# Kernel tuning notes

Measured on AMD Instinct MI355X. Metric: run time of the kernel, lower is better.

Reference implementation:

```python
import jax, jax.numpy as jnp
import numpy as np

B, F, D, V = 8192, 26, 32, 100000
H1, H2 = 128, 128  # cin_size
U1, U2 = 400, 400  # dnn hidden units


def setup_inputs() -> dict:
    key = jax.random.key(0)
    ks = jax.random.split(key, 12)
    s = 0.05  # keep activations/sigmoid in a sane range
    return {
        "dense_inputs": jax.random.normal(ks[0], (B, 13), jnp.float32),
        "sparse_inputs": jax.random.randint(ks[1], (B, F), 0, V, jnp.int32),
        "E": jax.random.normal(ks[2], (F, V, D), jnp.float32) * s,
        "W_cin0": jax.random.normal(ks[3], (F, F, H1), jnp.float32) * s,
        "W_cin1": jax.random.normal(ks[4], (F, H1, H2), jnp.float32) * s,
        "W1": jax.random.normal(ks[5], (F * D, U1), jnp.float32) * s,
        "b1": jnp.zeros((U1,), jnp.float32),
        "W2": jax.random.normal(ks[6], (U1, U2), jnp.float32) * s,
        "b2": jnp.zeros((U2,), jnp.float32),
        "w_lin": jax.random.normal(ks[7], (F, 1), jnp.float32) * s,
        "b_lin": jnp.zeros((1,), jnp.float32),
        "w_out": jax.random.normal(ks[8], (1 + H1 + H2 + U2 + 13, 1), jnp.float32) * s,
        "b_out": jnp.zeros((1,), jnp.float32),
    }


def reference(dense_inputs, sparse_inputs, E, W_cin0, W_cin1, W1, b1, W2, b2,
              w_lin, b_lin, w_out, b_out):
    # Linear part: Dense(1) applied to raw (cast) sparse ids, as in the TF code.
    linear_out = sparse_inputs.astype(jnp.float32) @ w_lin + b_lin  # [B,1]

    # Embedding lookup: per-field tables. embed[b,f,:] = E[f, sparse[b,f], :]
    embed = E[jnp.arange(F)[None, :], sparse_inputs]  # [B,F,D]

    # CIN. The split->matmul->reshape->conv1d chain is exactly:
    #   x_{k+1}[b,h,d] = sum_{i,j} W_k[i,j,h] * X0[b,i,d] * x_k[b,j,d]
    X0 = embed
    x1 = jnp.einsum('bid,bjd,ijh->bhd', X0, X0, W_cin0)   # [B,H1,D]
    x2 = jnp.einsum('bid,bjd,ijh->bhd', X0, x1, W_cin1)   # [B,H2,D]
    cin_out = jnp.concatenate([x1, x2], axis=1).sum(axis=-1)  # [B,H1+H2]

    # DNN on flattened embeddings (dropout rate 0 -> identity at inference).
    v = embed.reshape(B, F * D)
    h = jax.nn.relu(v @ W1 + b1)
    h = jax.nn.relu(h @ W2 + b2)  # [B,U2]

    total = jnp.concatenate([linear_out, cin_out, h, dense_inputs], axis=-1)
    return jax.nn.sigmoid(total @ w_out + b_out)  # [B,1]
```

## Files before the change

kernel.cpp:

```cpp
#include <hip/hip_runtime.h>
#include <hip/hip_bf16.h>
#include <math.h>

typedef __attribute__((ext_vector_type(8))) short bf16x8;
typedef __attribute__((ext_vector_type(4))) float f32x4;

#define B_ 8192
#define F_ 26
#define D_ 32
#define V_ 100000
#define NP_ 351
#define KP_ 352

static const size_t OFF_VB    = 0;
static const size_t OFF_LIN   = 13631488;
static const size_t OFF_CIN1  = 13664256;
static const size_t OFF_CIN2P = 17858560;
static const size_t OFF_G     = 34635776;
static const size_t OFF_H1B   = 89161728;
static const size_t OFF_H2    = 95715328;
static const size_t OFF_W0T   = 108822528;
static const size_t OFF_WC1T  = 108912640;
static const size_t OFF_W1T   = 109764608;
static const size_t OFF_W2T   = 110430208;

static __device__ __forceinline__ unsigned short f2b(float f) {
    unsigned int u = __float_as_uint(f);
    return (unsigned short)((u + 0x7FFF + ((u >> 16) & 1)) >> 16);
}
static __device__ __forceinline__ unsigned short f2bt(float f) {
    return (unsigned short)(__float_as_uint(f) >> 16);
}
static __device__ __forceinline__ unsigned int pk2t(float a, float b) {
    return __builtin_amdgcn_perm(__float_as_uint(b), __float_as_uint(a), 0x07060302u);
}
static __device__ __forceinline__ float bf2f(unsigned short u) {
    return __uint_as_float(((unsigned int)u) << 16);
}

static __device__ __forceinline__ void transpose_body(
    const float* __restrict__ src, unsigned short* __restrict__ dst,
    int K, int N, int bx, int by)
{
    __shared__ float tl[32][33];
    const int lx = threadIdx.x & 31, ly = threadIdx.x >> 5;
    const int n0 = bx * 32, k0 = by * 32;
#pragma unroll
    for (int i = 0; i < 4; ++i) {
        int k = k0 + ly + i * 8, n = n0 + lx;
        if (k < K && n < N) tl[ly + i * 8][lx] = src[(size_t)k * N + n];
    }
    __syncthreads();
#pragma unroll
    for (int i = 0; i < 4; ++i) {
        int n = n0 + ly + i * 8, k = k0 + lx;
        if (k < K && n < N) dst[(size_t)n * K + k] = f2b(tl[lx][ly + i * 8]);
    }
}

__global__ __launch_bounds__(256) void k0_all(
    const float* __restrict__ W0, const float* __restrict__ Wc1,
    const float* __restrict__ W1, const float* __restrict__ W2,
    unsigned short* __restrict__ W0t, unsigned short* __restrict__ Wc1t,
    unsigned short* __restrict__ W1t, unsigned short* __restrict__ W2t)
{
    int bid = blockIdx.x;
    if (bid < 176) {
        int g = bid * 256 + threadIdx.x;
        if (g < 128 * KP_) {
            int h = g / KP_, p = g % KP_;
            float w = 0.f;
            if (p < NP_) {
                int i = 0, base = 0;
                while (base + (F_ - i) <= p) { base += F_ - i; ++i; }
                int j = i + (p - base);
                w = W0[(i * F_ + j) * 128 + h];
                if (i != j) w += W0[(j * F_ + i) * 128 + h];
            }
            W0t[g] = f2b(w);
        }
        return;
    }
    bid -= 176;
    const float* src; unsigned short* dst; int K, N, nx;
    if (bid < 416)               { src = Wc1; dst = Wc1t; K = 3328; N = 128; nx = 4; }
    else if ((bid -= 416) < 338) { src = W1;  dst = W1t;  K = 832;  N = 400; nx = 13; }
    else                         { bid -= 338; src = W2; dst = W2t; K = 400; N = 400; nx = 13; }
    transpose_body(src, dst, K, N, bid % nx, bid / nx);
}

__global__ __launch_bounds__(256) void k1_embed_cin(
    const int*   __restrict__ sparse,
    const float* __restrict__ E,
    const unsigned short* __restrict__ W0t,
    const float* __restrict__ wlin,
    const float* __restrict__ blin,
    unsigned short* __restrict__ vb,
    float* __restrict__ lin,
    float* __restrict__ cin1,
    unsigned short* __restrict__ G)
{
    __shared__ __align__(16) unsigned short embB[32][40];
    __shared__ __align__(16) unsigned short P[32][360];
    __shared__ __align__(16) unsigned short x1s[128][40];
    __shared__ float cin1t[2][128];
    __shared__ float linb[F_];
    __shared__ int   idxs[F_];
    __shared__ unsigned char pI[KP_], pJ[KP_];

    const int b = blockIdx.x, t = threadIdx.x;

    if (t < F_) {
        int id = sparse[b * F_ + t];
        idxs[t] = id;
        linb[t] = (float)id * wlin[t];
        int i = t, base = F_ * i - (i * (i - 1)) / 2;
        for (int j = i; j < F_; ++j) { pI[base + j - i] = (unsigned char)i; pJ[base + j - i] = (unsigned char)j; }
    }
    __syncthreads();

    if (t < 208) {
        int f = t >> 3, q = t & 7;
        float4 r = *(const float4*)(E + ((size_t)f * V_ + idxs[f]) * D_ + q * 4);
        uint2 uu;
        uu.x = pk2t(r.x, r.y);
        uu.y = pk2t(r.z, r.w);
        *(uint2*)&embB[f][q * 4] = uu;
        *(uint2*)(vb + (size_t)b * 832 + f * 32 + q * 4) = uu;
    }
    if (t >= 208 && t < 208 + 96) {
        int o = t - 208;
        *(unsigned int*)&embB[26 + (o >> 4)][(o & 15) * 2] = 0u;
    }
    __syncthreads();

    {
        const int d = t & 31, pb = t >> 5;
        const int p0 = pb * 44;
        for (int k = 0; k < 22; ++k) {
            int p = p0 + 2 * k;
            float a  = bf2f(embB[pI[p]][d]) * bf2f(embB[pJ[p]][d]);
            float c2 = (p + 1 < NP_) ? bf2f(embB[pI[p + 1]][d]) * bf2f(embB[pJ[p + 1]][d]) : 0.f;
            *(unsigned int*)&P[d][p] = pk2t(a, c2);
        }
        if (t == 0) { float s = blin[0]; for (int f = 0; f < F_; ++f) s += linb[f]; lin[b] = s; }
    }
    __syncthreads();

    const int wave = t >> 6, lane = t & 63;
    const int lr = lane & 15, lg = lane >> 4;
    const int mt = wave & 1, ntb = (wave >> 1) * 4;
    f32x4 acc[4] = {};
    {
        const unsigned short* Arow = &P[mt * 16 + lr][lg * 8];
        for (int kt = 0; kt < 11; ++kt) {
            bf16x8 af = *(const bf16x8*)(Arow + kt * 32);
#pragma unroll
            for (int n = 0; n < 4; ++n) {
                const unsigned short* bp = W0t + (size_t)((ntb + n) * 16 + lr) * KP_ + kt * 32 + lg * 8;
                bf16x8 bfg = *(const bf16x8*)bp;
                acc[n] = __builtin_amdgcn_mfma_f32_16x16x32_bf16(af, bfg, acc[n], 0, 0, 0);
            }
        }
    }
#pragma unroll
    for (int n = 0; n < 4; ++n) {
        float s = acc[n][0] + acc[n][1] + acc[n][2] + acc[n][3];
        s += __shfl_xor(s, 16, 64);
        s += __shfl_xor(s, 32, 64);
        int h = (ntb + n) * 16 + lr;
        if (lg == 0) cin1t[mt][h] = s;
        int d0 = mt * 16 + lg * 4;
        *(unsigned int*)&x1s[h][d0]     = pk2t(acc[n][0], acc[n][1]);
        *(unsigned int*)&x1s[h][d0 + 2] = pk2t(acc[n][2], acc[n][3]);
    }
    __syncthreads();

    if (t < 128) cin1[(size_t)b * 128 + t] = cin1t[0][t] + cin1t[1][t];

    {
        bf16x8 ea = *(const bf16x8*)&embB[mt * 16 + lr][lg * 8];
#pragma unroll
        for (int n = 0; n < 4; ++n) {
            bf16x8 xb = *(const bf16x8*)&x1s[(ntb + n) * 16 + lr][lg * 8];
            f32x4 g = {};
            g = __builtin_amdgcn_mfma_f32_16x16x32_bf16(ea, xb, g, 0, 0, 0);
            int j = (ntb + n) * 16 + lr;
            int i0 = mt * 16 + lg * 4;
#pragma unroll
            for (int r = 0; r < 4; ++r) {
                int i = i0 + r;
                if (i < F_) G[(size_t)b * 3328 + i * 128 + j] = f2bt(g[r]);
            }
        }
    }
}

static __device__ __forceinline__ void gemm_body(
    const unsigned short* __restrict__ A, int lda, int kbase,
    const unsigned short* __restrict__ Bt, int ldb, int N,
    const float* __restrict__ bias, bool relu, bool outb,
    void* __restrict__ C, int ldc, int m0, int n0,
    unsigned short (*As)[40], unsigned short (*Bs)[40])
{
    const int t = threadIdx.x;
    const int wave = t >> 6, lane = t & 63;
    const int lr = lane & 15, lg = lane >> 4;
    const int wn = wave * 32;
    const int ar = t >> 2, kg = (t & 3) * 8;

    const unsigned short* aptr = A  + (size_t)(m0 + ar) * lda + kbase + kg;
    const unsigned short* bp0  = Bt + (size_t)(n0 + ar) * ldb + kbase + kg;
    const unsigned short* bp1  = Bt + (size_t)(n0 + 64 + ar) * ldb + kbase + kg;
    const bool bn0 = (n0 + ar) < N, bn1 = (n0 + 64 + ar) < N;

    const uint4 z4 = make_uint4(0u, 0u, 0u, 0u);
    uint4 av  = *(const uint4*)aptr;
    uint4 bv0 = bn0 ? *(const uint4*)bp0 : z4;
    uint4 bv1 = bn1 ? *(const uint4*)bp1 : z4;

    f32x4 acc[4][2] = {};
    for (int kt = 0; kt < 26; ++kt) {
        *(uint4*)&As[ar][kg]      = av;
        *(uint4*)&Bs[ar][kg]      = bv0;
        *(uint4*)&Bs[64 + ar][kg] = bv1;
        __syncthreads();
        if (kt + 1 < 26) {
            av  = *(const uint4*)(aptr + (kt + 1) * 32);
            bv0 = bn0 ? *(const uint4*)(bp0 + (kt + 1) * 32) : z4;
            bv1 = bn1 ? *(const uint4*)(bp1 + (kt + 1) * 32) : z4;
        }
        bf16x8 af[4], bfr[2];
#pragma unroll
        for (int i = 0; i < 4; ++i) af[i]  = *(const bf16x8*)&As[i * 16 + lr][lg * 8];
#pragma unroll
        for (int j = 0; j < 2; ++j) bfr[j] = *(const bf16x8*)&Bs[wn + j * 16 + lr][lg * 8];
#pragma unroll
        for (int i = 0; i < 4; ++i)
#pragma unroll
            for (int j = 0; j < 2; ++j)
                acc[i][j] = __builtin_amdgcn_mfma_f32_16x16x32_bf16(af[i], bfr[j], acc[i][j], 0, 0, 0);
        __syncthreads();
    }
#pragma unroll
    for (int i = 0; i < 4; ++i) {
        int mrow = m0 + i * 16 + lg * 4;
#pragma unroll
        for (int j = 0; j < 2; ++j) {
            int col = n0 + wn + j * 16 + lr;
            if (col >= N) continue;
            float bb = bias ? bias[col] : 0.f;
#pragma unroll
            for (int r = 0; r < 4; ++r) {
                float vv = acc[i][j][r] + bb;
                if (relu) vv = fmaxf(vv, 0.f);
                if (outb) ((unsigned short*)C)[(size_t)(mrow + r) * ldc + col] = f2bt(vv);
                else      ((float*)C)[(size_t)(mrow + r) * ldc + col] = vv;
            }
        }
    }
}

__global__ __launch_bounds__(256) void k2_h1_cin2(
    const unsigned short* __restrict__ vb, const unsigned short* __restrict__ W1t,
    const float* __restrict__ b1, unsigned short* __restrict__ h1b,
    const unsigned short* __restrict__ G, const unsigned short* __restrict__ Wc1t,
    float* __restrict__ cin2p)
{
    __shared__ __align__(16) unsigned short As[64][40];
    __shared__ __align__(16) unsigned short Bs[128][40];
    const int m0 = blockIdx.y * 64;
    if (blockIdx.z == 0) {
        gemm_body(vb, 832, 0, W1t, 832, 400, b1, true, true, h1b, 400,
                  m0, blockIdx.x * 128, As, Bs);
    } else {
        float* Cp = cin2p + (size_t)blockIdx.x * B_ * 128;
        gemm_body(G, 3328, blockIdx.x * 832, Wc1t, 3328, 128, nullptr, false, false, Cp, 128,
                  m0, 0, As, Bs);
    }
}

__global__ __launch_bounds__(256) void k2_h2(
    const unsigned short* __restrict__ A, const unsigned short* __restrict__ Bt,
    const float* __restrict__ bias, float* __restrict__ C)
{
    __shared__ __align__(16) unsigned short As[64][40];
    __shared__ __align__(16) unsigned short Bs[128][40];
    const int t = threadIdx.x;
    const int m0 = blockIdx.y * 64, n0 = blockIdx.x * 128;
    const int N = 400, K = 400, ld = 400;
    const int wave = t >> 6, lane = t & 63;
    const int lr = lane & 15, lg = lane >> 4;
    const int wn = wave * 32;
    const int ar = t >> 2, kg = (t & 3) * 8;

    const unsigned short* aptr = A  + (size_t)(m0 + ar) * ld + kg;
    const unsigned short* bp0  = Bt + (size_t)(n0 + ar) * ld + kg;
    const unsigned short* bp1  = Bt + (size_t)(n0 + 64 + ar) * ld + kg;
    const bool bn0 = (n0 + ar) < N, bn1 = (n0 + 64 + ar) < N;
    const uint4 z4 = make_uint4(0u, 0u, 0u, 0u);
    uint4 av, bv0, bv1;
    av  = (kg < K)        ? *(const uint4*)aptr : z4;
    bv0 = (bn0 && kg < K) ? *(const uint4*)bp0  : z4;
    bv1 = (bn1 && kg < K) ? *(const uint4*)bp1  : z4;

    f32x4 acc[4][2] = {};
    const int nkt = 13;
    for (int kt = 0; kt < nkt; ++kt) {
        *(uint4*)&As[ar][kg]      = av;
        *(uint4*)&Bs[ar][kg]      = bv0;
        *(uint4*)&Bs[64 + ar][kg] = bv1;
        __syncthreads();
        int kn = (kt + 1) * 32 + kg;
        if (kt + 1 < nkt) {
            av  = (kn < K)        ? *(const uint4*)(aptr + (kt + 1) * 32) : z4;
            bv0 = (bn0 && kn < K) ? *(const uint4*)(bp0  + (kt + 1) * 32) : z4;
            bv1 = (bn1 && kn < K) ? *(const uint4*)(bp1  + (kt + 1) * 32) : z4;
        }
        bf16x8 af[4], bfr[2];
#pragma unroll
        for (int i = 0; i < 4; ++i) af[i]  = *(const bf16x8*)&As[i * 16 + lr][lg * 8];
#pragma unroll
        for (int j = 0; j < 2; ++j) bfr[j] = *(const bf16x8*)&Bs[wn + j * 16 + lr][lg * 8];
#pragma unroll
        for (int i = 0; i < 4; ++i)
#pragma unroll
            for (int j = 0; j < 2; ++j)
                acc[i][j] = __builtin_amdgcn_mfma_f32_16x16x32_bf16(af[i], bfr[j], acc[i][j], 0, 0, 0);
        __syncthreads();
    }
#pragma unroll
    for (int i = 0; i < 4; ++i) {
        int mrow = m0 + i * 16 + lg * 4;
#pragma unroll
        for (int j = 0; j < 2; ++j) {
            int col = n0 + wn + j * 16 + lr;
            if (col >= N) continue;
            float bb = bias[col];
#pragma unroll
            for (int r = 0; r < 4; ++r)
                C[(size_t)(mrow + r) * N + col] = fmaxf(acc[i][j][r] + bb, 0.f);
        }
    }
}

__global__ __launch_bounds__(256) void k3_final(
    const float* __restrict__ lin,
    const float* __restrict__ cin1,
    const float* __restrict__ cin2p,
    const float* __restrict__ h2,
    const float* __restrict__ dense,
    const float* __restrict__ wout,
    const float* __restrict__ bout,
    float* __restrict__ out)
{
    const int wave = threadIdx.x >> 6, lane = threadIdx.x & 63;
    const int b = blockIdx.x * 4 + wave;
    const size_t S = (size_t)B_ * 128;
    float s = 0.f;
    for (int o = lane; o < 670; o += 64) {
        float f;
        if (o == 0)        f = lin[b];
        else if (o < 129)  f = cin1[(size_t)b * 128 + (o - 1)];
        else if (o < 257) {
            size_t idx = (size_t)b * 128 + (o - 129);
            f = (cin2p[idx] + cin2p[S + idx]) + (cin2p[2 * S + idx] + cin2p[3 * S + idx]);
        }
        else if (o < 657)  f = h2[(size_t)b * 400 + (o - 257)];
        else               f = dense[(size_t)b * 13 + (o - 657)];
        s = fmaf(f, wout[o], s);
    }
#pragma unroll
    for (int off = 32; off > 0; off >>= 1) s += __shfl_down(s, off, 64);
    if (lane == 0) out[b] = 1.f / (1.f + expf(-(s + bout[0])));
}

extern "C" void kernel_launch(void* const* d_in, const int* in_sizes, int n_in,
                              void* d_out, int out_size, void* d_ws, size_t ws_size,
                              hipStream_t stream) {
    const float* dense  = (const float*)d_in[0];
    const int*   sparse = (const int*)  d_in[1];
    const float* E      = (const float*)d_in[2];
    const float* W0     = (const float*)d_in[3];
    const float* Wc1    = (const float*)d_in[4];
    const float* W1     = (const float*)d_in[5];
    const float* b1     = (const float*)d_in[6];
    const float* W2     = (const float*)d_in[7];
    const float* b2     = (const float*)d_in[8];
    const float* wlin   = (const float*)d_in[9];
    const float* blin   = (const float*)d_in[10];
    const float* wout   = (const float*)d_in[11];
    const float* bout   = (const float*)d_in[12];
    float* out = (float*)d_out;

    char* ws = (char*)d_ws;
    unsigned short* vb    = (unsigned short*)(ws + OFF_VB);
    float*          lin   = (float*)(ws + OFF_LIN);
    float*          cin1  = (float*)(ws + OFF_CIN1);
    float*          cin2p = (float*)(ws + OFF_CIN2P);
    unsigned short* G     = (unsigned short*)(ws + OFF_G);
    unsigned short* h1b   = (unsigned short*)(ws + OFF_H1B);
    float*          h2    = (float*)(ws + OFF_H2);
    unsigned short* W0t   = (unsigned short*)(ws + OFF_W0T);
    unsigned short* Wc1t  = (unsigned short*)(ws + OFF_WC1T);
    unsigned short* W1t   = (unsigned short*)(ws + OFF_W1T);
    unsigned short* W2t   = (unsigned short*)(ws + OFF_W2T);

    k0_all<<<176 + 416 + 338 + 169, 256, 0, stream>>>(W0, Wc1, W1, W2, W0t, Wc1t, W1t, W2t);
    k1_embed_cin<<<B_, 256, 0, stream>>>(sparse, E, W0t, wlin, blin, vb, lin, cin1, G);
    k2_h1_cin2<<<dim3(4, 128, 2), 256, 0, stream>>>(vb, W1t, b1, h1b, G, Wc1t, cin2p);
    k2_h2<<<dim3(4, 128), 256, 0, stream>>>(h1b, W2t, b2, h2);
    k3_final<<<B_ / 4, 256, 0, stream>>>(lin, cin1, cin2p, h2, dense, wout, bout, out);
}
```

Before: 561.1 us.

## Fuse output-layer dot products into GEMM epilogues and batch two samples per CIN block

```diff
diff --git a/kernel.cpp b/kernel.cpp
--- a/kernel.cpp
+++ b/kernel.cpp
@@ -12,17 +12,16 @@
 #define NP_ 351
 #define KP_ 352
 
-static const size_t OFF_VB    = 0;
-static const size_t OFF_LIN   = 13631488;
-static const size_t OFF_CIN1  = 13664256;
-static const size_t OFF_CIN2P = 17858560;
-static const size_t OFF_G     = 34635776;
-static const size_t OFF_H1B   = 89161728;
-static const size_t OFF_H2    = 95715328;
-static const size_t OFF_W0T   = 108822528;
-static const size_t OFF_WC1T  = 108912640;
-static const size_t OFF_W1T   = 109764608;
-static const size_t OFF_W2T   = 110430208;
+static const size_t OFF_VB   = 0;
+static const size_t OFF_FD0  = 13631488;
+static const size_t OFF_PDC2 = 13664256;
+static const size_t OFF_PDH2 = 13795328;
+static const size_t OFF_G    = 13926400;
+static const size_t OFF_H1B  = 68452352;
+static const size_t OFF_W0T  = 75005952;
+static const size_t OFF_WC1T = 75096064;
+static const size_t OFF_W1T  = 75948032;
+static const size_t OFF_W2T  = 76613632;
 
 static __device__ __forceinline__ unsigned short f2b(float f) {
     unsigned int u = __float_as_uint(f);
@@ -95,113 +94,141 @@
     const unsigned short* __restrict__ W0t,
     const float* __restrict__ wlin,
     const float* __restrict__ blin,
+    const float* __restrict__ wout,
     unsigned short* __restrict__ vb,
-    float* __restrict__ lin,
-    float* __restrict__ cin1,
+    float* __restrict__ fdot0,
     unsigned short* __restrict__ G)
 {
-    __shared__ __align__(16) unsigned short embB[32][40];
-    __shared__ __align__(16) unsigned short P[32][360];
-    __shared__ __align__(16) unsigned short x1s[128][40];
-    __shared__ float cin1t[2][128];
-    __shared__ float linb[F_];
-    __shared__ int   idxs[F_];
-    __shared__ unsigned char pI[KP_], pJ[KP_];
-
-    const int b = blockIdx.x, t = threadIdx.x;
-
+    __shared__ __align__(16) unsigned short embB[64][40];
+    __shared__ __align__(16) unsigned short Pbuf[64 * 360];
+    __shared__ float wdot[4];
+    __shared__ float linv[52];
+    __shared__ int   idxs[52];
+    __shared__ unsigned char pI[NP_], pJ[NP_];
+
+    const int b0 = blockIdx.x * 2, t = threadIdx.x;
+
+    if (t < 52) {
+        int bb = t >= 26 ? 1 : 0, ff = t - bb * 26;
+        int id = sparse[(b0 + bb) * F_ + ff];
+        idxs[t] = id;
+        linv[t] = (float)id * wlin[ff];
+    }
     if (t < F_) {
-        int id = sparse[b * F_ + t];
-        idxs[t] = id;
-        linb[t] = (float)id * wlin[t];
         int i = t, base = F_ * i - (i * (i - 1)) / 2;
         for (int j = i; j < F_; ++j) { pI[base + j - i] = (unsigned char)i; pJ[base + j - i] = (unsigned char)j; }
     }
     __syncthreads();
 
-    if (t < 208) {
-        int f = t >> 3, q = t & 7;
-        float4 r = *(const float4*)(E + ((size_t)f * V_ + idxs[f]) * D_ + q * 4);
-        uint2 uu;
-        uu.x = pk2t(r.x, r.y);
-        uu.y = pk2t(r.z, r.w);
-        *(uint2*)&embB[f][q * 4] = uu;
-        *(uint2*)(vb + (size_t)b * 832 + f * 32 + q * 4) = uu;
-    }
-    if (t >= 208 && t < 208 + 96) {
-        int o = t - 208;
-        *(unsigned int*)&embB[26 + (o >> 4)][(o & 15) * 2] = 0u;
+    for (int r = t; r < 416; r += 256) {
+        int f = r >> 3, q = r & 7;
+        int bb = f >= 26 ? 1 : 0, ff = f - bb * 26;
+        float4 v4 = *(const float4*)(E + ((size_t)ff * V_ + idxs[f]) * D_ + q * 4);
+        uint2 uu; uu.x = pk2t(v4.x, v4.y); uu.y = pk2t(v4.z, v4.w);
+        *(uint2*)&embB[bb * 32 + ff][q * 4] = uu;
+        *(uint2*)(vb + (size_t)(b0 + bb) * 832 + ff * 32 + q * 4) = uu;
+    }
+    if (t < 192) {
+        int row = t >> 4, bb = row >= 6 ? 1 : 0, rr = row - bb * 6;
+        *(unsigned int*)&embB[bb * 32 + 26 + rr][(t & 15) * 2] = 0u;
     }
     __syncthreads();
 
     {
-        const int d = t & 31, pb = t >> 5;
-        const int p0 = pb * 44;
-        for (int k = 0; k < 22; ++k) {
+        const int d = t & 31, sub = t >> 5;
+        const int bb = sub & 1, pb = sub >> 1;
+        const int e0 = bb * 32;
+        const int p0 = pb * 88;
+        unsigned short* Prow = &Pbuf[(e0 + d) * 360];
+        for (int k = 0; k < 44; ++k) {
             int p = p0 + 2 * k;
-            float a  = bf2f(embB[pI[p]][d]) * bf2f(embB[pJ[p]][d]);
-            float c2 = (p + 1 < NP_) ? bf2f(embB[pI[p + 1]][d]) * bf2f(embB[pJ[p + 1]][d]) : 0.f;
-            *(unsigned int*)&P[d][p] = pk2t(a, c2);
-        }
-        if (t == 0) { float s = blin[0]; for (int f = 0; f < F_; ++f) s += linb[f]; lin[b] = s; }
+            float a = bf2f(embB[e0 + pI[p]][d]) * bf2f(embB[e0 + pJ[p]][d]);
+            float c = (p + 1 < NP_) ? bf2f(embB[e0 + pI[p + 1]][d]) * bf2f(embB[e0 + pJ[p + 1]][d]) : 0.f;
+            *(unsigned int*)&Prow[p] = pk2t(a, c);
+        }
     }
     __syncthreads();
 
     const int wave = t >> 6, lane = t & 63;
     const int lr = lane & 15, lg = lane >> 4;
-    const int mt = wave & 1, ntb = (wave >> 1) * 4;
-    f32x4 acc[4] = {};
+    const int bb = wave & 1;
+    const int h0 = (wave >> 1) * 64;
+    f32x4 acc[2][4] = {};
     {
-        const unsigned short* Arow = &P[mt * 16 + lr][lg * 8];
+        const unsigned short* Ab = &Pbuf[(bb * 32 + lr) * 360];
+        const unsigned short* Bb = W0t + (size_t)(h0 + lr) * KP_ + lg * 8;
         for (int kt = 0; kt < 11; ++kt) {
-            bf16x8 af = *(const bf16x8*)(Arow + kt * 32);
+            const int ko = kt * 32 + lg * 8;
+            bf16x8 a0 = *(const bf16x8*)(Ab + ko);
+            bf16x8 a1 = *(const bf16x8*)(Ab + 16 * 360 + ko);
 #pragma unroll
             for (int n = 0; n < 4; ++n) {
-                const unsigned short* bp = W0t + (size_t)((ntb + n) * 16 + lr) * KP_ + kt * 32 + lg * 8;
-                bf16x8 bfg = *(const bf16x8*)bp;
-                acc[n] = __builtin_amdgcn_mfma_f32_16x16x32_bf16(af, bfg, acc[n], 0, 0, 0);
-            }
-        }
-    }
+                bf16x8 bw = *(const bf16x8*)(Bb + (size_t)(n * 16) * KP_ + kt * 32);
+                acc[0][n] = __builtin_amdgcn_mfma_f32_16x16x32_bf16(a0, bw, acc[0][n], 0, 0, 0);
+                acc[1][n] = __builtin_amdgcn_mfma_f32_16x16x32_bf16(a1, bw, acc[1][n], 0, 0, 0);
+            }
+        }
+    }
+
+    float dotv = 0.f;
 #pragma unroll
     for (int n = 0; n < 4; ++n) {
-        float s = acc[n][0] + acc[n][1] + acc[n][2] + acc[n][3];
+        float s = acc[0][n][0] + acc[0][n][1] + acc[0][n][2] + acc[0][n][3]
+                + acc[1][n][0] + acc[1][n][1] + acc[1][n][2] + acc[1][n][3];
         s += __shfl_xor(s, 16, 64);
         s += __shfl_xor(s, 32, 64);
-        int h = (ntb + n) * 16 + lr;
-        if (lg == 0) cin1t[mt][h] = s;
-        int d0 = mt * 16 + lg * 4;
-        *(unsigned int*)&x1s[h][d0]     = pk2t(acc[n][0], acc[n][1]);
-        *(unsigned int*)&x1s[h][d0 + 2] = pk2t(acc[n][2], acc[n][3]);
-    }
-    __syncthreads();
-
-    if (t < 128) cin1[(size_t)b * 128 + t] = cin1t[0][t] + cin1t[1][t];
+        if (lg == 0) dotv += s * wout[1 + h0 + n * 16 + lr];
+    }
+#pragma unroll
+    for (int off = 1; off <= 32; off <<= 1) dotv += __shfl_xor(dotv, off, 64);
+    if (lane == 0) wdot[wave] = dotv;
+    __syncthreads();
+
+#pragma unroll
+    for (int n = 0; n < 4; ++n) {
+        const int base = ((bb << 7) + h0 + n * 16 + lr) * 40;
+#pragma unroll
+        for (int mi = 0; mi < 2; ++mi) {
+            *(unsigned int*)&Pbuf[base + mi * 16 + lg * 4]     = pk2t(acc[mi][n][0], acc[mi][n][1]);
+            *(unsigned int*)&Pbuf[base + mi * 16 + lg * 4 + 2] = pk2t(acc[mi][n][2], acc[mi][n][3]);
+        }
+    }
+    __syncthreads();
+
+    if (t < 2) {
+        float s = blin[0];
+        for (int f = 0; f < F_; ++f) s += linv[t * 26 + f];
+        fdot0[b0 + t] = s * wout[0] + wdot[t] + wdot[t + 2];
+    }
 
     {
-        bf16x8 ea = *(const bf16x8*)&embB[mt * 16 + lr][lg * 8];
+        bf16x8 ga0 = *(const bf16x8*)&embB[bb * 32 + lr][lg * 8];
+        bf16x8 ga1 = *(const bf16x8*)&embB[bb * 32 + 16 + lr][lg * 8];
+        unsigned short* Gb = G + (size_t)(b0 + bb) * 3328;
 #pragma unroll
         for (int n = 0; n < 4; ++n) {
-            bf16x8 xb = *(const bf16x8*)&x1s[(ntb + n) * 16 + lr][lg * 8];
-            f32x4 g = {};
-            g = __builtin_amdgcn_mfma_f32_16x16x32_bf16(ea, xb, g, 0, 0, 0);
-            int j = (ntb + n) * 16 + lr;
-            int i0 = mt * 16 + lg * 4;
+            const int j = h0 + n * 16 + lr;
+            bf16x8 xb = *(const bf16x8*)&Pbuf[((bb << 7) + j) * 40 + lg * 8];
+            f32x4 g0 = {}, g1 = {};
+            g0 = __builtin_amdgcn_mfma_f32_16x16x32_bf16(ga0, xb, g0, 0, 0, 0);
+            g1 = __builtin_amdgcn_mfma_f32_16x16x32_bf16(ga1, xb, g1, 0, 0, 0);
 #pragma unroll
             for (int r = 0; r < 4; ++r) {
-                int i = i0 + r;
-                if (i < F_) G[(size_t)b * 3328 + i * 128 + j] = f2bt(g[r]);
-            }
-        }
-    }
-}
-
-static __device__ __forceinline__ void gemm_body(
-    const unsigned short* __restrict__ A, int lda, int kbase,
+                int i0 = lg * 4 + r;
+                Gb[i0 * 128 + j] = f2bt(g0[r]);
+                int i1 = 16 + lg * 4 + r;
+                if (i1 < F_) Gb[i1 * 128 + j] = f2bt(g1[r]);
+            }
+        }
+    }
+}
+
+static __device__ __forceinline__ void gemm_core(
+    const unsigned short* __restrict__ A, int lda,
     const unsigned short* __restrict__ Bt, int ldb, int N,
-    const float* __restrict__ bias, bool relu, bool outb,
-    void* __restrict__ C, int ldc, int m0, int n0,
-    unsigned short (*As)[40], unsigned short (*Bs)[40])
+    int m0, int n0, int kbase, int kend,
+    unsigned short (*As)[40], unsigned short (*Bs)[40],
+    f32x4 (*acc)[2])
 {
     const int t = threadIdx.x;
     const int wave = t >> 6, lane = t & 63;
@@ -213,109 +240,25 @@
     const unsigned short* bp0  = Bt + (size_t)(n0 + ar) * ldb + kbase + kg;
     const unsigned short* bp1  = Bt + (size_t)(n0 + 64 + ar) * ldb + kbase + kg;
     const bool bn0 = (n0 + ar) < N, bn1 = (n0 + 64 + ar) < N;
-
     const uint4 z4 = make_uint4(0u, 0u, 0u, 0u);
-    uint4 av  = *(const uint4*)aptr;
-    uint4 bv0 = bn0 ? *(const uint4*)bp0 : z4;
-    uint4 bv1 = bn1 ? *(const uint4*)bp1 : z4;
-
-    f32x4 acc[4][2] = {};
-    for (int kt = 0; kt < 26; ++kt) {
-        *(uint4*)&As[ar][kg]      = av;
-        *(uint4*)&Bs[ar][kg]      = bv0;
-        *(uint4*)&Bs[64 + ar][kg] = bv1;
-        __syncthreads();
-        if (kt + 1 < 26) {
-            av  = *(const uint4*)(aptr + (kt + 1) * 32);
-            bv0 = bn0 ? *(const uint4*)(bp0 + (kt + 1) * 32) : z4;
-            bv1 = bn1 ? *(const uint4*)(bp1 + (kt + 1) * 32) : z4;
-        }
-        bf16x8 af[4], bfr[2];
-#pragma unroll
-        for (int i = 0; i < 4; ++i) af[i]  = *(const bf16x8*)&As[i * 16 + lr][lg * 8];
-#pragma unroll
-        for (int j = 0; j < 2; ++j) bfr[j] = *(const bf16x8*)&Bs[wn + j * 16 + lr][lg * 8];
-#pragma unroll
-        for (int i = 0; i < 4; ++i)
-#pragma unroll
-            for (int j = 0; j < 2; ++j)
-                acc[i][j] = __builtin_amdgcn_mfma_f32_16x16x32_bf16(af[i], bfr[j], acc[i][j], 0, 0, 0);
-        __syncthreads();
-    }
-#pragma unroll
-    for (int i = 0; i < 4; ++i) {
-        int mrow = m0 + i * 16 + lg * 4;
-#pragma unroll
-        for (int j = 0; j < 2; ++j) {
-            int col = n0 + wn + j * 16 + lr;
-            if (col >= N) continue;
-            float bb = bias ? bias[col] : 0.f;
-#pragma unroll
-            for (int r = 0; r < 4; ++r) {
-                float vv = acc[i][j][r] + bb;
-                if (relu) vv = fmaxf(vv, 0.f);
-                if (outb) ((unsigned short*)C)[(size_t)(mrow + r) * ldc + col] = f2bt(vv);
-                else      ((float*)C)[(size_t)(mrow + r) * ldc + col] = vv;
-            }
-        }
-    }
-}
-
-__global__ __launch_bounds__(256) void k2_h1_cin2(
-    const unsigned short* __restrict__ vb, const unsigned short* __restrict__ W1t,
-    const float* __restrict__ b1, unsigned short* __restrict__ h1b,
-    const unsigned short* __restrict__ G, const unsigned short* __restrict__ Wc1t,
-    float* __restrict__ cin2p)
-{
-    __shared__ __align__(16) unsigned short As[64][40];
-    __shared__ __align__(16) unsigned short Bs[128][40];
-    const int m0 = blockIdx.y * 64;
-    if (blockIdx.z == 0) {
-        gemm_body(vb, 832, 0, W1t, 832, 400, b1, true, true, h1b, 400,
-                  m0, blockIdx.x * 128, As, Bs);
-    } else {
-        float* Cp = cin2p + (size_t)blockIdx.x * B_ * 128;
-        gemm_body(G, 3328, blockIdx.x * 832, Wc1t, 3328, 128, nullptr, false, false, Cp, 128,
-                  m0, 0, As, Bs);
-    }
-}
-
-__global__ __launch_bounds__(256) void k2_h2(
-    const unsigned short* __restrict__ A, const unsigned short* __restrict__ Bt,
-    const float* __restrict__ bias, float* __restrict__ C)
-{
-    __shared__ __align__(16) unsigned short As[64][40];
-    __shared__ __align__(16) unsigned short Bs[128][40];
-    const int t = threadIdx.x;
-    const int m0 = blockIdx.y * 64, n0 = blockIdx.x * 128;
-    const int N = 400, K = 400, ld = 400;
-    const int wave = t >> 6, lane = t & 63;
-    const int lr = lane & 15, lg = lane >> 4;
-    const int wn = wave * 32;
-    const int ar = t >> 2, kg = (t & 3) * 8;
-
-    const unsigned short* aptr = A  + (size_t)(m0 + ar) * ld + kg;
-    const unsigned short* bp0  = Bt + (size_t)(n0 + ar) * ld + kg;
-    const unsigned short* bp1  = Bt + (size_t)(n0 + 64 + ar) * ld + kg;
-    const bool bn0 = (n0 + ar) < N, bn1 = (n0 + 64 + ar) < N;
-    const uint4 z4 = make_uint4(0u, 0u, 0u, 0u);
+    const int nkt = (kend - kbase + 31) >> 5;
     uint4 av, bv0, bv1;
-    av  = (kg < K)        ? *(const uint4*)aptr : z4;
-    bv0 = (bn0 && kg < K) ? *(const uint4*)bp0  : z4;
-    bv1 = (bn1 && kg < K) ? *(const uint4*)bp1  : z4;
-
-    f32x4 acc[4][2] = {};
-    const int nkt = 13;
+    {
+        int k = kbase + kg;
+        av  = (k < kend)        ? *(const uint4*)aptr : z4;
+        bv0 = (bn0 && k < kend) ? *(const uint4*)bp0  : z4;
+        bv1 = (bn1 && k < kend) ? *(const uint4*)bp1  : z4;
+    }
     for (int kt = 0; kt < nkt; ++kt) {
         *(uint4*)&As[ar][kg]      = av;
         *(uint4*)&Bs[ar][kg]      = bv0;
         *(uint4*)&Bs[64 + ar][kg] = bv1;
         __syncthreads();
-        int kn = (kt + 1) * 32 + kg;
         if (kt + 1 < nkt) {
-            av  = (kn < K)        ? *(const uint4*)(aptr + (kt + 1) * 32) : z4;
-            bv0 = (bn0 && kn < K) ? *(const uint4*)(bp0  + (kt + 1) * 32) : z4;
-            bv1 = (bn1 && kn < K) ? *(const uint4*)(bp1  + (kt + 1) * 32) : z4;
+            int kn = kbase + (kt + 1) * 32 + kg;
+            av  = (kn < kend)        ? *(const uint4*)(aptr + (kt + 1) * 32) : z4;
+            bv0 = (bn0 && kn < kend) ? *(const uint4*)(bp0  + (kt + 1) * 32) : z4;
+            bv1 = (bn1 && kn < kend) ? *(const uint4*)(bp1  + (kt + 1) * 32) : z4;
         }
         bf16x8 af[4], bfr[2];
 #pragma unroll
@@ -329,50 +272,124 @@
                 acc[i][j] = __builtin_amdgcn_mfma_f32_16x16x32_bf16(af[i], bfr[j], acc[i][j], 0, 0, 0);
         __syncthreads();
     }
-#pragma unroll
-    for (int i = 0; i < 4; ++i) {
-        int mrow = m0 + i * 16 + lg * 4;
-#pragma unroll
-        for (int j = 0; j < 2; ++j) {
-            int col = n0 + wn + j * 16 + lr;
-            if (col >= N) continue;
-            float bb = bias[col];
-#pragma unroll
-            for (int r = 0; r < 4; ++r)
-                C[(size_t)(mrow + r) * N + col] = fmaxf(acc[i][j][r] + bb, 0.f);
-        }
-    }
+}
+
+__global__ __launch_bounds__(256) void k2_h1_cin2(
+    const unsigned short* __restrict__ vb, const unsigned short* __restrict__ W1t,
+    const float* __restrict__ b1, unsigned short* __restrict__ h1b,
+    const unsigned short* __restrict__ G, const unsigned short* __restrict__ Wc1t,
+    const float* __restrict__ wout, float* __restrict__ pdc2)
+{
+    __shared__ __align__(16) unsigned short As[64][40];
+    __shared__ __align__(16) unsigned short Bs[128][40];
+    __shared__ float red[4][64];
+    const int t = threadIdx.x;
+    const int wave = t >> 6, lane = t & 63;
+    const int lr = lane & 15, lg = lane >> 4;
+    const int m0 = blockIdx.y * 64;
+    f32x4 acc[4][2] = {};
+
+    if (blockIdx.z == 0) {
+        const int n0 = blockIdx.x * 128;
+        gemm_core(vb, 832, W1t, 832, 400, m0, n0, 0, 832, As, Bs, acc);
+#pragma unroll
+        for (int i = 0; i < 4; ++i) {
+            int mrow = m0 + i * 16 + lg * 4;
+#pragma unroll
+            for (int j = 0; j < 2; ++j) {
+                int col = n0 + wave * 32 + j * 16 + lr;
+                if (col >= 400) continue;
+                float bb = b1[col];
+#pragma unroll
+                for (int r = 0; r < 4; ++r)
+                    h1b[(size_t)(mrow + r) * 400 + col] = f2bt(fmaxf(acc[i][j][r] + bb, 0.f));
+            }
+        }
+    } else {
+        const int chunk = blockIdx.x;
+        gemm_core(G, 3328, Wc1t, 3328, 128, m0, 0, chunk * 832, chunk * 832 + 832, As, Bs, acc);
+        float v[4][4];
+#pragma unroll
+        for (int i = 0; i < 4; ++i)
+#pragma unroll
+            for (int r = 0; r < 4; ++r) {
+                float s = 0.f;
+#pragma unroll
+                for (int j = 0; j < 2; ++j)
+                    s = fmaf(acc[i][j][r], wout[129 + wave * 32 + j * 16 + lr], s);
+#pragma unroll
+                for (int off = 1; off <= 8; off <<= 1) s += __shfl_xor(s, off, 64);
+                v[i][r] = s;
+            }
+        if (lr == 0) {
+#pragma unroll
+            for (int i = 0; i < 4; ++i)
+#pragma unroll
+                for (int r = 0; r < 4; ++r) red[wave][i * 16 + lg * 4 + r] = v[i][r];
+        }
+        __syncthreads();
+        if (t < 64) pdc2[(size_t)chunk * B_ + m0 + t] = red[0][t] + red[1][t] + red[2][t] + red[3][t];
+    }
+}
+
+__global__ __launch_bounds__(256) void k2_h2(
+    const unsigned short* __restrict__ h1b, const unsigned short* __restrict__ W2t,
+    const float* __restrict__ b2, const float* __restrict__ wout,
+    float* __restrict__ pdh2)
+{
+    __shared__ __align__(16) unsigned short As[64][40];
+    __shared__ __align__(16) unsigned short Bs[128][40];
+    __shared__ float red[4][64];
+    const int t = threadIdx.x;
+    const int wave = t >> 6, lane = t & 63;
+    const int lr = lane & 15, lg = lane >> 4;
+    const int m0 = blockIdx.y * 64, n0 = blockIdx.x * 128;
+    f32x4 acc[4][2] = {};
+    gemm_core(h1b, 400, W2t, 400, 400, m0, n0, 0, 400, As, Bs, acc);
+    float v[4][4];
+#pragma unroll
+    for (int i = 0; i < 4; ++i)
+#pragma unroll
+        for (int r = 0; r < 4; ++r) {
+            float s = 0.f;
+#pragma unroll
+            for (int j = 0; j < 2; ++j) {
+                int col = n0 + wave * 32 + j * 16 + lr;
+                if (col < 400)
+                    s = fmaf(fmaxf(acc[i][j][r] + b2[col], 0.f), wout[257 + col], s);
+            }
+#pragma unroll
+            for (int off = 1; off <= 8; off <<= 1) s += __shfl_xor(s, off, 64);
+            v[i][r] = s;
+        }
+    if (lr == 0) {
+#pragma unroll
+        for (int i = 0; i < 4; ++i)
+#pragma unroll
+            for (int r = 0; r < 4; ++r) red[wave][i * 16 + lg * 4 + r] = v[i][r];
+    }
+    __syncthreads();
+    if (t < 64) pdh2[(size_t)blockIdx.x * B_ + m0 + t] = red[0][t] + red[1][t] + red[2][t] + red[3][t];
 }
 
 __global__ __launch_bounds__(256) void k3_final(
-    const float* __restrict__ lin,
-    const float* __restrict__ cin1,
-    const float* __restrict__ cin2p,
-    const float* __restrict__ h2,
+    const float* __restrict__ fdot0,
+    const float* __restrict__ pdc2,
+    const float* __restrict__ pdh2,
     const float* __restrict__ dense,
     const float* __restrict__ wout,
     const float* __restrict__ bout,
     float* __restrict__ out)
 {
-    const int wave = threadIdx.x >> 6, lane = threadIdx.x & 63;
-    const int b = blockIdx.x * 4 + wave;
-    const size_t S = (size_t)B_ * 128;
-    float s = 0.f;
-    for (int o = lane; o < 670; o += 64) {
-        float f;
-        if (o == 0)        f = lin[b];
-        else if (o < 129)  f = cin1[(size_t)b * 128 + (o - 1)];
-        else if (o < 257) {
-            size_t idx = (size_t)b * 128 + (o - 129);
-            f = (cin2p[idx] + cin2p[S + idx]) + (cin2p[2 * S + idx] + cin2p[3 * S + idx]);
-        }
-        else if (o < 657)  f = h2[(size_t)b * 400 + (o - 257)];
-        else               f = dense[(size_t)b * 13 + (o - 657)];
-        s = fmaf(f, wout[o], s);
-    }
-#pragma unroll
-    for (int off = 32; off > 0; off >>= 1) s += __shfl_down(s, off, 64);
-    if (lane == 0) out[b] = 1.f / (1.f + expf(-(s + bout[0])));
+    const int b = blockIdx.x * 256 + threadIdx.x;
+    float s = fdot0[b];
+#pragma unroll
+    for (int z = 0; z < 4; ++z) s += pdc2[(size_t)z * B_ + b];
+#pragma unroll
+    for (int z = 0; z < 4; ++z) s += pdh2[(size_t)z * B_ + b];
+#pragma unroll
+    for (int q = 0; q < 13; ++q) s = fmaf(dense[(size_t)b * 13 + q], wout[657 + q], s);
+    out[b] = 1.f / (1.f + expf(-(s + bout[0])));
 }
 
 extern "C" void kernel_launch(void* const* d_in, const int* in_sizes, int n_in,
@@ -395,20 +412,19 @@
 
     char* ws = (char*)d_ws;
     unsigned short* vb    = (unsigned short*)(ws + OFF_VB);
-    float*          lin   = (float*)(ws + OFF_LIN);
-    float*          cin1  = (float*)(ws + OFF_CIN1);
-    float*          cin2p = (float*)(ws + OFF_CIN2P);
+    float*          fdot0 = (float*)(ws + OFF_FD0);
+    float*          pdc2  = (float*)(ws + OFF_PDC2);
+    float*          pdh2  = (float*)(ws + OFF_PDH2);
     unsigned short* G     = (unsigned short*)(ws + OFF_G);
     unsigned short* h1b   = (unsigned short*)(ws + OFF_H1B);
-    float*          h2    = (float*)(ws + OFF_H2);
     unsigned short* W0t   = (unsigned short*)(ws + OFF_W0T);
     unsigned short* Wc1t  = (unsigned short*)(ws + OFF_WC1T);
     unsigned short* W1t   = (unsigned short*)(ws + OFF_W1T);
     unsigned short* W2t   = (unsigned short*)(ws + OFF_W2T);
 
     k0_all<<<176 + 416 + 338 + 169, 256, 0, stream>>>(W0, Wc1, W1, W2, W0t, Wc1t, W1t, W2t);
-    k1_embed_cin<<<B_, 256, 0, stream>>>(sparse, E, W0t, wlin, blin, vb, lin, cin1, G);
-    k2_h1_cin2<<<dim3(4, 128, 2), 256, 0, stream>>>(vb, W1t, b1, h1b, G, Wc1t, cin2p);
-    k2_h2<<<dim3(4, 128), 256, 0, stream>>>(h1b, W2t, b2, h2);
-    k3_final<<<B_ / 4, 256, 0, stream>>>(lin, cin1, cin2p, h2, dense, wout, bout, out);
-}
+    k1_embed_cin<<<B_ / 2, 256, 0, stream>>>(sparse, E, W0t, wlin, blin, wout, vb, fdot0, G);
+    k2_h1_cin2<<<dim3(4, 128, 2), 256, 0, stream>>>(vb, W1t, b1, h1b, G, Wc1t, wout, pdc2);
+    k2_h2<<<dim3(4, 128), 256, 0, stream>>>(h1b, W2t, b2, wout, pdh2);
+    k3_final<<<B_ / 256, 256, 0, stream>>>(fdot0, pdc2, pdh2, dense, wout, bout, out);
+}
```

New measurement: 534.9 us. -4.7%, faster.
